# Kernel optimization log

Hardware: AMD Instinct MI355X
Metric: run time of the kernel (lower is better)

Reference implementation:

```python
import jax, jax.numpy as jnp
import numpy as np

QUERY_DIM = 512
KEY_DIM = 512
HIDDEN_DIM = 512


def setup_inputs() -> dict:
    key = jax.random.key(0)
    k1, k2, k3, k4, k5 = jax.random.split(key, 5)
    B, S = 32, 2048
    query = jax.random.normal(k1, (B, QUERY_DIM), dtype=jnp.float32)
    keys = jax.random.normal(k2, (B, S, KEY_DIM), dtype=jnp.float32)
    # nn.Linear weights stored as [out_features, in_features]
    Wq = jax.random.normal(k3, (HIDDEN_DIM, QUERY_DIM), dtype=jnp.float32) / np.sqrt(QUERY_DIM)
    Wk = jax.random.normal(k4, (HIDDEN_DIM, KEY_DIM), dtype=jnp.float32) / np.sqrt(KEY_DIM)
    w_att = jax.random.normal(k5, (HIDDEN_DIM,), dtype=jnp.float32) / np.sqrt(HIDDEN_DIM)
    return {"query": query, "keys": keys, "Wq": Wq, "Wk": Wk, "w_att": w_att}


def reference(query, keys, Wq, Wk, w_att):
    # values defaults to keys
    values = keys
    q = query @ Wq.T                               # [B, H]
    k = jnp.einsum('bsd,hd->bsh', keys, Wk)        # [B, S, H]
    combined = jnp.tanh(q[:, None, :] + k)         # [B, S, H]
    scores = jnp.einsum('bsh,h->bs', combined, w_att)  # [B, S]
    attn = jax.nn.softmax(scores, axis=-1)         # [B, S]
    out = jnp.einsum('bs,bsd->bd', attn, values)   # [B, D]
    return (out, attn)
```

## Files before the change

kernel.cpp:

```cpp
#include <hip/hip_runtime.h>
#include <hip/hip_fp16.h>

typedef _Float16 f16x8 __attribute__((ext_vector_type(8)));
typedef float f32x4 __attribute__((ext_vector_type(4)));

#define WS_QV 0
#define WS_BF 65536
#define WS_SC 589824
#define WS_VP 851968

__global__ __launch_bounds__(256) void prep_kernel(
    const float* __restrict__ query, const float* __restrict__ Wq,
    const float* __restrict__ Wk, float* __restrict__ qv,
    _Float16* __restrict__ bfrag) {
  const int blk = blockIdx.x, tid = threadIdx.x;
  if (blk < 64) {
    const int b = blk >> 1;
    const int h = ((blk & 1) << 8) + tid;
    const float4* qr = (const float4*)(query + (size_t)b * 512);
    const float4* wr = (const float4*)(Wq + (size_t)h * 512);
    float acc = 0.f;
#pragma unroll 8
    for (int i = 0; i < 128; ++i) {
      float4 a = qr[i], w = wr[i];
      acc += a.x * w.x + a.y * w.y + a.z * w.z + a.w * w.w;
    }
    qv[b * 512 + h] = acc;
  } else {
    const int u = (blk - 64) * 4 + (tid >> 6);
    const int l = tid & 63;
    const int col = ((u >> 4) << 4) + (l & 15);
    const int k0 = ((u & 15) << 5) + ((l >> 4) << 3);
    const float4* src = (const float4*)(Wk + (size_t)col * 512 + k0);
    float4 x = src[0], y = src[1];
    f16x8 v;
    v[0] = (_Float16)x.x; v[1] = (_Float16)x.y;
    v[2] = (_Float16)x.z; v[3] = (_Float16)x.w;
    v[4] = (_Float16)y.x; v[5] = (_Float16)y.y;
    v[6] = (_Float16)y.z; v[7] = (_Float16)y.w;
    *(f16x8*)(bfrag + (size_t)u * 512 + l * 8) = v;
  }
}

__global__ __launch_bounds__(256, 2) void scores_kernel(
    const float* __restrict__ keys, const _Float16* __restrict__ bfrag,
    const float* __restrict__ qv, const float* __restrict__ w_att,
    float* __restrict__ scores) {
  __shared__ __align__(128) unsigned char lds[32768];
  const int tid = threadIdx.x, w = tid >> 6, l = tid & 63;
  const int row0 = blockIdx.x * 64;
  const int b = row0 >> 11;

  const int sr = tid >> 2, scb = tid & 3;
  const float* gsrc = keys + (size_t)(row0 + sr) * 512 + scb * 32;
  const int wbase = sr * 256 + scb * 64;
  const int wswz = (sr & 7) << 4;

  float4 stg[8];
#pragma unroll
  for (int j = 0; j < 8; ++j) stg[j] = ((const float4*)gsrc)[j];
  {
    unsigned char* dbuf = lds;
#pragma unroll
    for (int j2 = 0; j2 < 4; ++j2) {
      float4 x = stg[2 * j2], y = stg[2 * j2 + 1];
      f16x8 h;
      h[0] = (_Float16)x.x; h[1] = (_Float16)x.y;
      h[2] = (_Float16)x.z; h[3] = (_Float16)x.w;
      h[4] = (_Float16)y.x; h[5] = (_Float16)y.y;
      h[6] = (_Float16)y.z; h[7] = (_Float16)y.w;
      *(f16x8*)(dbuf + ((wbase + j2 * 16) ^ wswz)) = h;
    }
  }
  __syncthreads();

  f32x4 acc[4][8];
#pragma unroll
  for (int mt = 0; mt < 4; ++mt)
#pragma unroll
    for (int nt = 0; nt < 8; ++nt) {
      acc[mt][nt][0] = 0.f; acc[mt][nt][1] = 0.f;
      acc[mt][nt][2] = 0.f; acc[mt][nt][3] = 0.f;
    }

  const int aswz = (l & 7) << 4;
  const int arow = (l & 15) * 256;
  const int acol = (l >> 4) << 4;

#pragma unroll
  for (int c = 0; c < 4; ++c) {
    if (c < 3) {
      const float4* g = (const float4*)(gsrc + (c + 1) * 128);
#pragma unroll
      for (int j = 0; j < 8; ++j) stg[j] = g[j];
    }
    __builtin_amdgcn_sched_barrier(0);

    const unsigned char* buf = lds + (c & 1) * 16384;
#pragma unroll
    for (int kl = 0; kl < 4; ++kl) {
      const int ks = c * 4 + kl;
      f16x8 bf[8];
#pragma unroll
      for (int nt = 0; nt < 8; ++nt) {
        int u = (w * 8 + nt) * 16 + ks;
        bf[nt] = *(const f16x8*)(bfrag + (size_t)u * 512 + l * 8);
      }
      f16x8 af[4];
#pragma unroll
      for (int mt = 0; mt < 4; ++mt) {
        int byte = mt * 4096 + arow + ((kl * 64 + acol) ^ aswz);
        af[mt] = *(const f16x8*)(buf + byte);
      }
#pragma unroll
      for (int mt = 0; mt < 4; ++mt)
#pragma unroll
        for (int nt = 0; nt < 8; ++nt)
          acc[mt][nt] = __builtin_amdgcn_mfma_f32_16x16x32_f16(
              af[mt], bf[nt], acc[mt][nt], 0, 0, 0);
    }
    __builtin_amdgcn_sched_barrier(0);

    if (c < 3) {
      unsigned char* dbuf = lds + ((c + 1) & 1) * 16384;
#pragma unroll
      for (int j2 = 0; j2 < 4; ++j2) {
        float4 x = stg[2 * j2], y = stg[2 * j2 + 1];
        f16x8 h;
        h[0] = (_Float16)x.x; h[1] = (_Float16)x.y;
        h[2] = (_Float16)x.z; h[3] = (_Float16)x.w;
        h[4] = (_Float16)y.x; h[5] = (_Float16)y.y;
        h[6] = (_Float16)y.z; h[7] = (_Float16)y.w;
        *(f16x8*)(dbuf + ((wbase + j2 * 16) ^ wswz)) = h;
      }
    }
    __syncthreads();
  }

  float rs[16];
#pragma unroll
  for (int i = 0; i < 16; ++i) rs[i] = 0.f;
  const int hb = w * 128;
#pragma unroll
  for (int nt = 0; nt < 8; ++nt) {
    const int h = hb + nt * 16 + (l & 15);
    const float q = qv[b * 512 + h];
    const float wa = w_att[h];
#pragma unroll
    for (int mt = 0; mt < 4; ++mt)
#pragma unroll
      for (int r = 0; r < 4; ++r) {
        float x = q + acc[mt][nt][r];
        float e = __expf(x + x);
        float t = 1.f - __fdividef(2.f, e + 1.f);
        rs[mt * 4 + r] = __builtin_fmaf(t, wa, rs[mt * 4 + r]);
      }
  }
#pragma unroll
  for (int st = 1; st <= 8; st <<= 1)
#pragma unroll
    for (int i = 0; i < 16; ++i)
      rs[i] += __shfl_xor(rs[i], st, 64);

  __syncthreads();
  float* spart = (float*)lds;
  {
    const int idx = l & 15;
    float v = rs[0];
#pragma unroll
    for (int i = 1; i < 16; ++i) v = (idx == i) ? rs[i] : v;
    const int rrow = ((idx >> 2) << 4) + ((l >> 4) << 2) + (idx & 3);
    spart[w * 64 + rrow] = v;
  }
  __syncthreads();
  if (tid < 64) {
    float s = spart[tid] + spart[64 + tid] + spart[128 + tid] + spart[192 + tid];
    scores[row0 + tid] = s;
  }
}

__global__ __launch_bounds__(256) void out_kernel(
    const float* __restrict__ keys, const float* __restrict__ scores,
    float* __restrict__ attn_out, float* __restrict__ vpart) {
  __shared__ float red_mx[4], red_se[4];
  __shared__ float4 comb[128];
  const int tid = threadIdx.x;
  const int b = blockIdx.x >> 5;
  const int sc = blockIdx.x & 31;
  const float* srow = scores + (size_t)b * 2048;

  float sv[8];
  float mx = -1e30f;
#pragma unroll
  for (int i = 0; i < 8; ++i) { sv[i] = srow[i * 256 + tid]; mx = fmaxf(mx, sv[i]); }
#pragma unroll
  for (int st = 32; st >= 1; st >>= 1) mx = fmaxf(mx, __shfl_xor(mx, st, 64));
  if ((tid & 63) == 0) red_mx[tid >> 6] = mx;
  __syncthreads();
  mx = fmaxf(fmaxf(red_mx[0], red_mx[1]), fmaxf(red_mx[2], red_mx[3]));

  float se = 0.f;
#pragma unroll
  for (int i = 0; i < 8; ++i) se += __expf(sv[i] - mx);
#pragma unroll
  for (int st = 32; st >= 1; st >>= 1) se += __shfl_xor(se, st, 64);
  if ((tid & 63) == 0) red_se[tid >> 6] = se;
  __syncthreads();
  se = red_se[0] + red_se[1] + red_se[2] + red_se[3];
  const float rinv = 1.f / se;

  if (tid < 64) {
    int s = sc * 64 + tid;
    attn_out[(size_t)b * 2048 + s] = __expf(srow[s] - mx) * rinv;
  }

  const int c4 = tid & 127, rg = tid >> 7;
  const float4* kb4 = (const float4*)(keys + ((size_t)(b * 2048 + sc * 64 + rg * 32)) * 512);
  float4 a; a.x = 0.f; a.y = 0.f; a.z = 0.f; a.w = 0.f;
#pragma unroll 4
  for (int i = 0; i < 32; ++i) {
    float at = __expf(srow[sc * 64 + rg * 32 + i] - mx) * rinv;
    float4 kv = kb4[(size_t)i * 128 + c4];
    a.x = __builtin_fmaf(at, kv.x, a.x);
    a.y = __builtin_fmaf(at, kv.y, a.y);
    a.z = __builtin_fmaf(at, kv.z, a.z);
    a.w = __builtin_fmaf(at, kv.w, a.w);
  }
  if (rg) comb[c4] = a;
  __syncthreads();
  if (!rg) {
    float4 o = comb[c4];
    a.x += o.x; a.y += o.y; a.z += o.z; a.w += o.w;
    ((float4*)vpart)[(size_t)blockIdx.x * 128 + c4] = a;
  }
}

__global__ __launch_bounds__(256) void reduce_kernel(
    const float* __restrict__ vpart, float* __restrict__ out) {
  const int t = blockIdx.x * 256 + threadIdx.x;
  const int b = t >> 9, d = t & 511;
  float s = 0.f;
#pragma unroll
  for (int sc = 0; sc < 32; ++sc)
    s += vpart[((size_t)(b * 32 + sc)) * 512 + d];
  out[t] = s;
}

extern "C" void kernel_launch(void* const* d_in, const int* in_sizes, int n_in,
                              void* d_out, int out_size, void* d_ws, size_t ws_size,
                              hipStream_t stream) {
  const float* query = (const float*)d_in[0];
  const float* keys  = (const float*)d_in[1];
  const float* Wq    = (const float*)d_in[2];
  const float* Wk    = (const float*)d_in[3];
  const float* w_att = (const float*)d_in[4];
  float* out  = (float*)d_out;
  float* attn = out + 16384;
  char* ws = (char*)d_ws;
  float*    qv     = (float*)(ws + WS_QV);
  _Float16* bfrag  = (_Float16*)(ws + WS_BF);
  float*    scores = (float*)(ws + WS_SC);
  float*    vpart  = (float*)(ws + WS_VP);

  prep_kernel<<<192, 256, 0, stream>>>(query, Wq, Wk, qv, bfrag);
  scores_kernel<<<1024, 256, 0, stream>>>(keys, bfrag, qv, w_att, scores);
  out_kernel<<<1024, 256, 0, stream>>>(keys, scores, attn, vpart);
  reduce_kernel<<<64, 256, 0, stream>>>(vpart, out);
}
```

Before: 100.5 us.

## Fuse scores and weighted value sum with online-softmax partials in one pass

The scores kernel now keeps all four fp16 K chunks in a 64KB LDS buffer instead of double-buffering two. After computing a tile's scores, it takes a local max and exp, and accumulates the weighted sum of keys straight from LDS. It writes per-tile partial vectors plus max/sum stats, and a small combine kernel rescales them flash-style and also writes attn. This drops the second full fp32 read of keys and one launch. In exchange, the value accumulation uses fp16-rounded keys and the larger LDS footprint may reduce occupancy.

```diff
diff --git a/kernel.cpp b/kernel.cpp
--- a/kernel.cpp
+++ b/kernel.cpp
@@ -2,12 +2,14 @@
 #include <hip/hip_fp16.h>
 
 typedef _Float16 f16x8 __attribute__((ext_vector_type(8)));
+typedef _Float16 f16x2 __attribute__((ext_vector_type(2)));
 typedef float f32x4 __attribute__((ext_vector_type(4)));
 
 #define WS_QV 0
 #define WS_BF 65536
 #define WS_SC 589824
 #define WS_VP 851968
+#define WS_ST 2949120
 
 __global__ __launch_bounds__(256) void prep_kernel(
     const float* __restrict__ query, const float* __restrict__ Wq,
@@ -42,13 +44,18 @@
   }
 }
 
-__global__ __launch_bounds__(256, 2) void scores_kernel(
+__global__ __launch_bounds__(256, 2) void fused_kernel(
     const float* __restrict__ keys, const _Float16* __restrict__ bfrag,
     const float* __restrict__ qv, const float* __restrict__ w_att,
-    float* __restrict__ scores) {
-  __shared__ __align__(128) unsigned char lds[32768];
+    float* __restrict__ scores, float* __restrict__ vpart,
+    float* __restrict__ stats) {
+  __shared__ __align__(128) unsigned char lds[65536];
+  __shared__ float spart[256];
+  __shared__ float pb[64];
+  __shared__ float pb2[64];
   const int tid = threadIdx.x, w = tid >> 6, l = tid & 63;
-  const int row0 = blockIdx.x * 64;
+  const int wg = blockIdx.x;
+  const int row0 = wg * 64;
   const int b = row0 >> 11;
 
   const int sr = tid >> 2, scb = tid & 3;
@@ -96,7 +103,7 @@
     }
     __builtin_amdgcn_sched_barrier(0);
 
-    const unsigned char* buf = lds + (c & 1) * 16384;
+    const unsigned char* buf = lds + c * 16384;
 #pragma unroll
     for (int kl = 0; kl < 4; ++kl) {
       const int ks = c * 4 + kl;
@@ -122,7 +129,7 @@
     __builtin_amdgcn_sched_barrier(0);
 
     if (c < 3) {
-      unsigned char* dbuf = lds + ((c + 1) & 1) * 16384;
+      unsigned char* dbuf = lds + (c + 1) * 16384;
 #pragma unroll
       for (int j2 = 0; j2 < 4; ++j2) {
         float4 x = stg[2 * j2], y = stg[2 * j2 + 1];
@@ -133,8 +140,8 @@
         h[6] = (_Float16)y.z; h[7] = (_Float16)y.w;
         *(f16x8*)(dbuf + ((wbase + j2 * 16) ^ wswz)) = h;
       }
-    }
-    __syncthreads();
+      __syncthreads();
+    }
   }
 
   float rs[16];
@@ -162,8 +169,6 @@
     for (int i = 0; i < 16; ++i)
       rs[i] += __shfl_xor(rs[i], st, 64);
 
-  __syncthreads();
-  float* spart = (float*)lds;
   {
     const int idx = l & 15;
     float v = rs[0];
@@ -176,74 +181,76 @@
   if (tid < 64) {
     float s = spart[tid] + spart[64 + tid] + spart[128 + tid] + spart[192 + tid];
     scores[row0 + tid] = s;
-  }
-}
-
-__global__ __launch_bounds__(256) void out_kernel(
-    const float* __restrict__ keys, const float* __restrict__ scores,
-    float* __restrict__ attn_out, float* __restrict__ vpart) {
-  __shared__ float red_mx[4], red_se[4];
-  __shared__ float4 comb[128];
-  const int tid = threadIdx.x;
-  const int b = blockIdx.x >> 5;
-  const int sc = blockIdx.x & 31;
-  const float* srow = scores + (size_t)b * 2048;
-
-  float sv[8];
-  float mx = -1e30f;
-#pragma unroll
-  for (int i = 0; i < 8; ++i) { sv[i] = srow[i * 256 + tid]; mx = fmaxf(mx, sv[i]); }
-#pragma unroll
-  for (int st = 32; st >= 1; st >>= 1) mx = fmaxf(mx, __shfl_xor(mx, st, 64));
-  if ((tid & 63) == 0) red_mx[tid >> 6] = mx;
-  __syncthreads();
-  mx = fmaxf(fmaxf(red_mx[0], red_mx[1]), fmaxf(red_mx[2], red_mx[3]));
-
-  float se = 0.f;
-#pragma unroll
-  for (int i = 0; i < 8; ++i) se += __expf(sv[i] - mx);
-#pragma unroll
-  for (int st = 32; st >= 1; st >>= 1) se += __shfl_xor(se, st, 64);
-  if ((tid & 63) == 0) red_se[tid >> 6] = se;
-  __syncthreads();
-  se = red_se[0] + red_se[1] + red_se[2] + red_se[3];
-  const float rinv = 1.f / se;
-
-  if (tid < 64) {
-    int s = sc * 64 + tid;
-    attn_out[(size_t)b * 2048 + s] = __expf(srow[s] - mx) * rinv;
-  }
-
-  const int c4 = tid & 127, rg = tid >> 7;
-  const float4* kb4 = (const float4*)(keys + ((size_t)(b * 2048 + sc * 64 + rg * 32)) * 512);
-  float4 a; a.x = 0.f; a.y = 0.f; a.z = 0.f; a.w = 0.f;
-#pragma unroll 4
-  for (int i = 0; i < 32; ++i) {
-    float at = __expf(srow[sc * 64 + rg * 32 + i] - mx) * rinv;
-    float4 kv = kb4[(size_t)i * 128 + c4];
-    a.x = __builtin_fmaf(at, kv.x, a.x);
-    a.y = __builtin_fmaf(at, kv.y, a.y);
-    a.z = __builtin_fmaf(at, kv.z, a.z);
-    a.w = __builtin_fmaf(at, kv.w, a.w);
-  }
-  if (rg) comb[c4] = a;
-  __syncthreads();
-  if (!rg) {
-    float4 o = comb[c4];
-    a.x += o.x; a.y += o.y; a.z += o.z; a.w += o.w;
-    ((float4*)vpart)[(size_t)blockIdx.x * 128 + c4] = a;
-  }
-}
-
-__global__ __launch_bounds__(256) void reduce_kernel(
-    const float* __restrict__ vpart, float* __restrict__ out) {
-  const int t = blockIdx.x * 256 + threadIdx.x;
-  const int b = t >> 9, d = t & 511;
-  float s = 0.f;
-#pragma unroll
-  for (int sc = 0; sc < 32; ++sc)
-    s += vpart[((size_t)(b * 32 + sc)) * 512 + d];
-  out[t] = s;
+    pb[tid] = s;
+  }
+  __syncthreads();
+
+  float m = -1e30f;
+#pragma unroll 16
+  for (int r = 0; r < 64; ++r) m = fmaxf(m, pb[r]);
+  if (tid < 64) pb2[tid] = __expf(pb[tid] - m);
+  __syncthreads();
+
+  {
+    float a0 = 0.f, a1 = 0.f;
+    const unsigned char* q = lds + w * 16384;
+#pragma unroll 8
+    for (int r = 0; r < 64; ++r) {
+      f16x2 kv = *(const f16x2*)(q + r * 256 + ((4 * l) ^ ((r & 7) << 4)));
+      float p = pb2[r];
+      a0 = __builtin_fmaf(p, (float)kv[0], a0);
+      a1 = __builtin_fmaf(p, (float)kv[1], a1);
+    }
+    float2 o; o.x = a0; o.y = a1;
+    *(float2*)(vpart + (size_t)wg * 512 + 2 * tid) = o;
+  }
+  if (tid == 0) {
+    float lsum = 0.f;
+#pragma unroll 16
+    for (int r = 0; r < 64; ++r) lsum += pb2[r];
+    stats[wg * 2] = m;
+    stats[wg * 2 + 1] = lsum;
+  }
+}
+
+__global__ __launch_bounds__(256) void combine_kernel(
+    const float* __restrict__ vpart, const float* __restrict__ stats,
+    const float* __restrict__ scores, float* __restrict__ out,
+    float* __restrict__ attn) {
+  const int blk = blockIdx.x, tid = threadIdx.x;
+  const int b = blk & 31;
+  float mt[32], lt[32];
+  float M = -1e30f;
+#pragma unroll
+  for (int t = 0; t < 32; ++t) {
+    mt[t] = stats[(b * 32 + t) * 2];
+    lt[t] = stats[(b * 32 + t) * 2 + 1];
+    M = fmaxf(M, mt[t]);
+  }
+  float L = 0.f;
+#pragma unroll
+  for (int t = 0; t < 32; ++t) L += __expf(mt[t] - M) * lt[t];
+  const float rinv = 1.f / L;
+
+  if (blk < 32) {
+    const int d0 = 2 * tid;
+    float a0 = 0.f, a1 = 0.f;
+#pragma unroll
+    for (int t = 0; t < 32; ++t) {
+      float wgt = __expf(mt[t] - M);
+      float2 vp = *(const float2*)(vpart + ((size_t)(b * 32 + t)) * 512 + d0);
+      a0 = __builtin_fmaf(wgt, vp.x, a0);
+      a1 = __builtin_fmaf(wgt, vp.y, a1);
+    }
+    out[b * 512 + d0] = a0 * rinv;
+    out[b * 512 + d0 + 1] = a1 * rinv;
+  } else {
+#pragma unroll
+    for (int j = 0; j < 8; ++j) {
+      int s = j * 256 + tid;
+      attn[(size_t)b * 2048 + s] = __expf(scores[(size_t)b * 2048 + s] - M) * rinv;
+    }
+  }
 }
 
 extern "C" void kernel_launch(void* const* d_in, const int* in_sizes, int n_in,
@@ -261,9 +268,9 @@
   _Float16* bfrag  = (_Float16*)(ws + WS_BF);
   float*    scores = (float*)(ws + WS_SC);
   float*    vpart  = (float*)(ws + WS_VP);
+  float*    stats  = (float*)(ws + WS_ST);
 
   prep_kernel<<<192, 256, 0, stream>>>(query, Wq, Wk, qv, bfrag);
-  scores_kernel<<<1024, 256, 0, stream>>>(keys, bfrag, qv, w_att, scores);
-  out_kernel<<<1024, 256, 0, stream>>>(keys, scores, attn, vpart);
-  reduce_kernel<<<64, 256, 0, stream>>>(vpart, out);
-}
+  fused_kernel<<<1024, 256, 0, stream>>>(keys, bfrag, qv, w_att, scores, vpart, stats);
+  combine_kernel<<<64, 256, 0, stream>>>(vpart, stats, scores, out, attn);
+}
```

Measured after the change: 91.04 us. 1.1x faster.

## Split hidden dim across blocks, use 512-thread GEMM tiles, cache softmax exps in LDS

Applied to the files above, without the earlier changes.

The scores GEMM is retiled. Each block now handles 64 rows by 256 hidden columns with 8 waves in a 2x4 layout and a smaller K chunk of 64, and runs at higher occupancy. The two hidden halves write partial scores that the softmax kernel sums. The softmax/value kernel keeps the exponentials in LDS instead of recomputing them, and writes its partial outputs in fp16 to shrink traffic into the reduce kernel. The cost is that each keys tile is converted twice (once per hidden half), fp16 partials add rounding error, and more blocks are launched.

```diff
diff --git a/kernel.cpp b/kernel.cpp
--- a/kernel.cpp
+++ b/kernel.cpp
@@ -2,12 +2,13 @@
 #include <hip/hip_fp16.h>
 
 typedef _Float16 f16x8 __attribute__((ext_vector_type(8)));
+typedef _Float16 f16x4 __attribute__((ext_vector_type(4)));
 typedef float f32x4 __attribute__((ext_vector_type(4)));
 
 #define WS_QV 0
 #define WS_BF 65536
-#define WS_SC 589824
-#define WS_VP 851968
+#define WS_SP 589824
+#define WS_VP 1114112
 
 __global__ __launch_bounds__(256) void prep_kernel(
     const float* __restrict__ query, const float* __restrict__ Wq,
@@ -42,112 +43,107 @@
   }
 }
 
-__global__ __launch_bounds__(256, 2) void scores_kernel(
+__global__ __launch_bounds__(512, 4) void gemm_kernel(
     const float* __restrict__ keys, const _Float16* __restrict__ bfrag,
     const float* __restrict__ qv, const float* __restrict__ w_att,
-    float* __restrict__ scores) {
-  __shared__ __align__(128) unsigned char lds[32768];
+    float* __restrict__ spart_out) {
+  __shared__ __align__(128) unsigned char lds[16384];
+  __shared__ float sred[256];
   const int tid = threadIdx.x, w = tid >> 6, l = tid & 63;
-  const int row0 = blockIdx.x * 64;
+  const int bid = ((blockIdx.x & 7) << 8) + (blockIdx.x >> 3);
+  const int rt = bid >> 1, hs = bid & 1;
+  const int row0 = rt * 64;
   const int b = row0 >> 11;
-
-  const int sr = tid >> 2, scb = tid & 3;
-  const float* gsrc = keys + (size_t)(row0 + sr) * 512 + scb * 32;
-  const int wbase = sr * 256 + scb * 64;
+  const int wm = w >> 2, wn = w & 3;
+
+  const int sr = tid >> 3, sc8 = (tid & 7) << 3;
+  const float* gsrc = keys + (size_t)(row0 + sr) * 512 + sc8;
+  const int wbyte = sr * 128 + (sc8 << 1);
   const int wswz = (sr & 7) << 4;
 
-  float4 stg[8];
-#pragma unroll
-  for (int j = 0; j < 8; ++j) stg[j] = ((const float4*)gsrc)[j];
+  float4 stg[2];
+  stg[0] = ((const float4*)gsrc)[0];
+  stg[1] = ((const float4*)gsrc)[1];
   {
-    unsigned char* dbuf = lds;
-#pragma unroll
-    for (int j2 = 0; j2 < 4; ++j2) {
-      float4 x = stg[2 * j2], y = stg[2 * j2 + 1];
-      f16x8 h;
-      h[0] = (_Float16)x.x; h[1] = (_Float16)x.y;
-      h[2] = (_Float16)x.z; h[3] = (_Float16)x.w;
-      h[4] = (_Float16)y.x; h[5] = (_Float16)y.y;
-      h[6] = (_Float16)y.z; h[7] = (_Float16)y.w;
-      *(f16x8*)(dbuf + ((wbase + j2 * 16) ^ wswz)) = h;
-    }
-  }
-  __syncthreads();
-
-  f32x4 acc[4][8];
-#pragma unroll
-  for (int mt = 0; mt < 4; ++mt)
-#pragma unroll
-    for (int nt = 0; nt < 8; ++nt) {
+    f16x8 h;
+    h[0] = (_Float16)stg[0].x; h[1] = (_Float16)stg[0].y;
+    h[2] = (_Float16)stg[0].z; h[3] = (_Float16)stg[0].w;
+    h[4] = (_Float16)stg[1].x; h[5] = (_Float16)stg[1].y;
+    h[6] = (_Float16)stg[1].z; h[7] = (_Float16)stg[1].w;
+    *(f16x8*)(lds + (wbyte ^ wswz)) = h;
+  }
+  __syncthreads();
+
+  f32x4 acc[2][4];
+#pragma unroll
+  for (int mt = 0; mt < 2; ++mt)
+#pragma unroll
+    for (int nt = 0; nt < 4; ++nt) {
       acc[mt][nt][0] = 0.f; acc[mt][nt][1] = 0.f;
       acc[mt][nt][2] = 0.f; acc[mt][nt][3] = 0.f;
     }
 
   const int aswz = (l & 7) << 4;
-  const int arow = (l & 15) * 256;
-  const int acol = (l >> 4) << 4;
-
-#pragma unroll
-  for (int c = 0; c < 4; ++c) {
-    if (c < 3) {
-      const float4* g = (const float4*)(gsrc + (c + 1) * 128);
-#pragma unroll
-      for (int j = 0; j < 8; ++j) stg[j] = g[j];
+  const int akslot = (l >> 4) << 4;
+  const int arow = (wm * 32 + (l & 15)) * 128;
+
+#pragma unroll
+  for (int c = 0; c < 8; ++c) {
+    if (c < 7) {
+      const float4* g = (const float4*)(gsrc + (c + 1) * 64);
+      stg[0] = g[0]; stg[1] = g[1];
     }
     __builtin_amdgcn_sched_barrier(0);
 
-    const unsigned char* buf = lds + (c & 1) * 16384;
-#pragma unroll
-    for (int kl = 0; kl < 4; ++kl) {
-      const int ks = c * 4 + kl;
-      f16x8 bf[8];
-#pragma unroll
-      for (int nt = 0; nt < 8; ++nt) {
-        int u = (w * 8 + nt) * 16 + ks;
-        bf[nt] = *(const f16x8*)(bfrag + (size_t)u * 512 + l * 8);
+    const unsigned char* buf = lds + (c & 1) * 8192;
+#pragma unroll
+    for (int ks = 0; ks < 2; ++ks) {
+      const int KS = c * 2 + ks;
+      f16x8 af[2];
+#pragma unroll
+      for (int mt = 0; mt < 2; ++mt)
+        af[mt] = *(const f16x8*)(buf + arow + mt * 2048 +
+                                 ((ks * 64 + akslot) ^ aswz));
+#pragma unroll
+      for (int ng = 0; ng < 2; ++ng) {
+        f16x8 bf[2];
+#pragma unroll
+        for (int n2 = 0; n2 < 2; ++n2) {
+          const int u = ((hs << 4) + (wn << 2) + ng * 2 + n2) * 16 + KS;
+          bf[n2] = *(const f16x8*)(bfrag + (size_t)u * 512 + l * 8);
+        }
+#pragma unroll
+        for (int mt = 0; mt < 2; ++mt)
+#pragma unroll
+          for (int n2 = 0; n2 < 2; ++n2)
+            acc[mt][ng * 2 + n2] = __builtin_amdgcn_mfma_f32_16x16x32_f16(
+                af[mt], bf[n2], acc[mt][ng * 2 + n2], 0, 0, 0);
       }
-      f16x8 af[4];
-#pragma unroll
-      for (int mt = 0; mt < 4; ++mt) {
-        int byte = mt * 4096 + arow + ((kl * 64 + acol) ^ aswz);
-        af[mt] = *(const f16x8*)(buf + byte);
-      }
-#pragma unroll
-      for (int mt = 0; mt < 4; ++mt)
-#pragma unroll
-        for (int nt = 0; nt < 8; ++nt)
-          acc[mt][nt] = __builtin_amdgcn_mfma_f32_16x16x32_f16(
-              af[mt], bf[nt], acc[mt][nt], 0, 0, 0);
     }
     __builtin_amdgcn_sched_barrier(0);
 
-    if (c < 3) {
-      unsigned char* dbuf = lds + ((c + 1) & 1) * 16384;
-#pragma unroll
-      for (int j2 = 0; j2 < 4; ++j2) {
-        float4 x = stg[2 * j2], y = stg[2 * j2 + 1];
-        f16x8 h;
-        h[0] = (_Float16)x.x; h[1] = (_Float16)x.y;
-        h[2] = (_Float16)x.z; h[3] = (_Float16)x.w;
-        h[4] = (_Float16)y.x; h[5] = (_Float16)y.y;
-        h[6] = (_Float16)y.z; h[7] = (_Float16)y.w;
-        *(f16x8*)(dbuf + ((wbase + j2 * 16) ^ wswz)) = h;
-      }
+    if (c < 7) {
+      unsigned char* db = lds + ((c + 1) & 1) * 8192;
+      f16x8 h;
+      h[0] = (_Float16)stg[0].x; h[1] = (_Float16)stg[0].y;
+      h[2] = (_Float16)stg[0].z; h[3] = (_Float16)stg[0].w;
+      h[4] = (_Float16)stg[1].x; h[5] = (_Float16)stg[1].y;
+      h[6] = (_Float16)stg[1].z; h[7] = (_Float16)stg[1].w;
+      *(f16x8*)(db + (wbyte ^ wswz)) = h;
     }
     __syncthreads();
   }
 
-  float rs[16];
-#pragma unroll
-  for (int i = 0; i < 16; ++i) rs[i] = 0.f;
-  const int hb = w * 128;
-#pragma unroll
-  for (int nt = 0; nt < 8; ++nt) {
-    const int h = hb + nt * 16 + (l & 15);
+  float rs[8];
+#pragma unroll
+  for (int i = 0; i < 8; ++i) rs[i] = 0.f;
+#pragma unroll
+  for (int nt = 0; nt < 4; ++nt) {
+    const int h = (hs << 8) + (wn << 6) + (nt << 4) + (l & 15);
     const float q = qv[b * 512 + h];
     const float wa = w_att[h];
 #pragma unroll
-    for (int mt = 0; mt < 4; ++mt)
+    for (int mt = 0; mt < 2; ++mt)
 #pragma unroll
       for (int r = 0; r < 4; ++r) {
         float x = q + acc[mt][nt][r];
@@ -159,40 +155,46 @@
 #pragma unroll
   for (int st = 1; st <= 8; st <<= 1)
 #pragma unroll
-    for (int i = 0; i < 16; ++i)
+    for (int i = 0; i < 8; ++i)
       rs[i] += __shfl_xor(rs[i], st, 64);
 
-  __syncthreads();
-  float* spart = (float*)lds;
   {
     const int idx = l & 15;
-    float v = rs[0];
-#pragma unroll
-    for (int i = 1; i < 16; ++i) v = (idx == i) ? rs[i] : v;
-    const int rrow = ((idx >> 2) << 4) + ((l >> 4) << 2) + (idx & 3);
-    spart[w * 64 + rrow] = v;
+    if (idx < 8) {
+      float v = rs[0];
+#pragma unroll
+      for (int i = 1; i < 8; ++i) v = (idx == i) ? rs[i] : v;
+      const int rloc = ((idx >> 2) << 4) + ((l >> 4) << 2) + (idx & 3);
+      sred[w * 32 + rloc] = v;
+    }
   }
   __syncthreads();
   if (tid < 64) {
-    float s = spart[tid] + spart[64 + tid] + spart[128 + tid] + spart[192 + tid];
-    scores[row0 + tid] = s;
-  }
-}
-
-__global__ __launch_bounds__(256) void out_kernel(
-    const float* __restrict__ keys, const float* __restrict__ scores,
-    float* __restrict__ attn_out, float* __restrict__ vpart) {
+    const int wmq = tid >> 5, rl = tid & 31;
+    float s = sred[(wmq * 4 + 0) * 32 + rl] + sred[(wmq * 4 + 1) * 32 + rl] +
+              sred[(wmq * 4 + 2) * 32 + rl] + sred[(wmq * 4 + 3) * 32 + rl];
+    spart_out[hs * 65536 + row0 + tid] = s;
+  }
+}
+
+__global__ __launch_bounds__(256) void softv_kernel(
+    const float* __restrict__ keys, const float* __restrict__ spart,
+    float* __restrict__ attn, _Float16* __restrict__ vpart) {
+  __shared__ float pe[2048];
   __shared__ float red_mx[4], red_se[4];
   __shared__ float4 comb[128];
   const int tid = threadIdx.x;
-  const int b = blockIdx.x >> 5;
-  const int sc = blockIdx.x & 31;
-  const float* srow = scores + (size_t)b * 2048;
+  const int b = blockIdx.x >> 5, sc = blockIdx.x & 31;
+  const float* p0 = spart + (size_t)b * 2048;
+  const float* p1 = spart + 65536 + (size_t)b * 2048;
 
   float sv[8];
   float mx = -1e30f;
 #pragma unroll
-  for (int i = 0; i < 8; ++i) { sv[i] = srow[i * 256 + tid]; mx = fmaxf(mx, sv[i]); }
+  for (int i = 0; i < 8; ++i) {
+    sv[i] = p0[i * 256 + tid] + p1[i * 256 + tid];
+    mx = fmaxf(mx, sv[i]);
+  }
 #pragma unroll
   for (int st = 32; st >= 1; st >>= 1) mx = fmaxf(mx, __shfl_xor(mx, st, 64));
   if ((tid & 63) == 0) red_mx[tid >> 6] = mx;
@@ -201,7 +203,11 @@
 
   float se = 0.f;
 #pragma unroll
-  for (int i = 0; i < 8; ++i) se += __expf(sv[i] - mx);
+  for (int i = 0; i < 8; ++i) {
+    float e = __expf(sv[i] - mx);
+    pe[i * 256 + tid] = e;
+    se += e;
+  }
 #pragma unroll
   for (int st = 32; st >= 1; st >>= 1) se += __shfl_xor(se, st, 64);
   if ((tid & 63) == 0) red_se[tid >> 6] = se;
@@ -211,38 +217,42 @@
 
   if (tid < 64) {
     int s = sc * 64 + tid;
-    attn_out[(size_t)b * 2048 + s] = __expf(srow[s] - mx) * rinv;
+    attn[(size_t)b * 2048 + s] = pe[s] * rinv;
   }
 
   const int c4 = tid & 127, rg = tid >> 7;
-  const float4* kb4 = (const float4*)(keys + ((size_t)(b * 2048 + sc * 64 + rg * 32)) * 512);
+  const float4* kb = (const float4*)(keys + ((size_t)(b * 2048 + sc * 64 + rg * 32)) * 512);
   float4 a; a.x = 0.f; a.y = 0.f; a.z = 0.f; a.w = 0.f;
 #pragma unroll 4
   for (int i = 0; i < 32; ++i) {
-    float at = __expf(srow[sc * 64 + rg * 32 + i] - mx) * rinv;
-    float4 kv = kb4[(size_t)i * 128 + c4];
-    a.x = __builtin_fmaf(at, kv.x, a.x);
-    a.y = __builtin_fmaf(at, kv.y, a.y);
-    a.z = __builtin_fmaf(at, kv.z, a.z);
-    a.w = __builtin_fmaf(at, kv.w, a.w);
+    float p = pe[sc * 64 + rg * 32 + i];
+    float4 kv = kb[(size_t)i * 128 + c4];
+    a.x = __builtin_fmaf(p, kv.x, a.x);
+    a.y = __builtin_fmaf(p, kv.y, a.y);
+    a.z = __builtin_fmaf(p, kv.z, a.z);
+    a.w = __builtin_fmaf(p, kv.w, a.w);
   }
   if (rg) comb[c4] = a;
   __syncthreads();
   if (!rg) {
     float4 o = comb[c4];
-    a.x += o.x; a.y += o.y; a.z += o.z; a.w += o.w;
-    ((float4*)vpart)[(size_t)blockIdx.x * 128 + c4] = a;
+    f16x4 h;
+    h[0] = (_Float16)((a.x + o.x) * rinv);
+    h[1] = (_Float16)((a.y + o.y) * rinv);
+    h[2] = (_Float16)((a.z + o.z) * rinv);
+    h[3] = (_Float16)((a.w + o.w) * rinv);
+    *(f16x4*)(vpart + (size_t)blockIdx.x * 512 + c4 * 4) = h;
   }
 }
 
 __global__ __launch_bounds__(256) void reduce_kernel(
-    const float* __restrict__ vpart, float* __restrict__ out) {
+    const _Float16* __restrict__ vpart, float* __restrict__ out) {
   const int t = blockIdx.x * 256 + threadIdx.x;
   const int b = t >> 9, d = t & 511;
   float s = 0.f;
 #pragma unroll
   for (int sc = 0; sc < 32; ++sc)
-    s += vpart[((size_t)(b * 32 + sc)) * 512 + d];
+    s += (float)vpart[((size_t)(b * 32 + sc)) * 512 + d];
   out[t] = s;
 }
 
@@ -259,11 +269,11 @@
   char* ws = (char*)d_ws;
   float*    qv     = (float*)(ws + WS_QV);
   _Float16* bfrag  = (_Float16*)(ws + WS_BF);
-  float*    scores = (float*)(ws + WS_SC);
-  float*    vpart  = (float*)(ws + WS_VP);
+  float*    spart  = (float*)(ws + WS_SP);
+  _Float16* vpart  = (_Float16*)(ws + WS_VP);
 
   prep_kernel<<<192, 256, 0, stream>>>(query, Wq, Wk, qv, bfrag);
-  scores_kernel<<<1024, 256, 0, stream>>>(keys, bfrag, qv, w_att, scores);
-  out_kernel<<<1024, 256, 0, stream>>>(keys, scores, attn, vpart);
+  gemm_kernel<<<2048, 512, 0, stream>>>(keys, bfrag, qv, w_att, spart);
+  softv_kernel<<<1024, 256, 0, stream>>>(keys, spart, attn, vpart);
   reduce_kernel<<<64, 256, 0, stream>>>(vpart, out);
 }
```

Result: slower. 113.6 us (+13.1%).
